# Performance work log

Hardware: AMD Instinct MI355X
Metric: run time of the kernel (lower is better)

Reference implementation:

```python
import jax, jax.numpy as jnp
import numpy as np

CP_SPACING = (4, 4, 4)
SIGMAS = tuple(0.44 * cp for cp in CP_SPACING)


def _gaussian_kernel_3d(sigmas):
    # Faithful to DeepReg layer_util.gaussian_filter_3d
    ks = [int(np.ceil(s * 3) + np.mod(np.ceil(s * 3) + 1, 2)) for s in sigmas]
    grid = np.stack(np.meshgrid(*[np.arange(k) for k in ks], indexing="ij"), axis=0)  # [3,k,k,k]
    mean = ((np.asarray(ks, np.float64) - 1.0) / 2.0).reshape(-1, 1, 1, 1)
    var = (np.asarray(sigmas, np.float64) ** 2.0).reshape(-1, 1, 1, 1)
    norm = 1.0 / (np.sqrt(2.0 * np.pi) ** 3 + np.prod(sigmas))  # as in DeepReg source
    kernel = norm * np.exp(-np.sum((grid - mean) ** 2.0 / (2.0 * var), axis=0))
    kernel = kernel / np.sum(kernel)  # sums to 1
    return kernel.astype(np.float32)  # [k,k,k]


def setup_inputs() -> dict:
    key = jax.random.key(0)
    image = jax.random.normal(key, (4, 160, 160, 160, 3), dtype=jnp.float32)  # DDF volume, 3 channels
    kernel = jnp.asarray(_gaussian_kernel_3d(SIGMAS))  # deterministic [7,7,7] Gaussian buffer
    return {"image": image, "kernel": kernel}


def reference(image, kernel):
    b, d1, d2, d3, c = image.shape
    # DeepReg's [k,k,k,3,3] diagonal kernel == depthwise blur per channel.
    kdw = jnp.tile(kernel[..., None, None], (1, 1, 1, 1, c))  # [k,k,k,1,C]
    blurred = jax.lax.conv_general_dilated(
        image, kdw,
        window_strides=(1, 1, 1),
        padding="SAME",
        dimension_numbers=("NDHWC", "DHWIO", "NDHWC"),
        feature_group_count=c,
    )
    # output control-point grid: ceil(dim / cp_spacing) + 3
    size = tuple(int(np.ceil(v / cp)) + 3 for v, cp in zip((d1, d2, d3), CP_SPACING))
    # tf.image.resize bilinear (TF2) uses half-pixel centers == jax.image.resize 'linear'
    out = jax.image.resize(blurred, (b,) + size + (c,), method="linear")
    return out
```

## Files before the change

### kernel.cpp

```cpp
#include <hip/hip_runtime.h>

#define NB 4
#define NI 160
#define NO 43
#define NC 3
#define KS 7
#define KPAD 3
#define MT 16
#define CH 8

#define ROWF (NI * NC)
#define PROW 132
#define PROW4 (PROW / 4)
#define LROW 484
#define SLICE (NO * NO * NC)

#define A1_BYTES ((size_t)NB * NI * NI * PROW * 4)
#define A2_BYTES ((size_t)NB * NI * NO * PROW * 4)
#define P2_THREADS ((size_t)NB * NI * NO * PROW4)
#define P3_THREADS ((size_t)NB * NO * NO * PROW4)

struct __align__(16) Tables {
    float wa3[NO][20];
    float w1[NO][MT];
    int   o1[NO][MT];
    int   o0[NO][MT];
    int   j3[NO];
    int   jlo[NO];
};

constexpr double ctaylor(double r) {
    double s = 1.0, term = 1.0;
    for (int n = 1; n <= 13; ++n) { term *= r / (double)n; s += term; }
    return s;
}
constexpr double cexp_neg(double x) {
    double y = -x;
    int k = (int)(y * 16.0);
    double r = y - (double)k / 16.0;
    double e16 = ctaylor(1.0 / 16.0);
    double p = 1.0;
    for (int i = 0; i < k; ++i) p *= e16;
    return 1.0 / (p * ctaylor(r));
}
constexpr int cceil(double x)  { int c = (int)x; return ((double)c < x) ? c + 1 : c; }
constexpr int cfloor(double x) { int f = (int)x; return ((double)f > x) ? f - 1 : f; }
constexpr double cabsd(double x) { return x < 0 ? -x : x; }

constexpr double comp_w(int j, double sf, int ilo, int ihi, const double* g) {
    if (j >= NI || j < 0) return 0.0;
    double cw = 0.0;
    for (int t = 0; t < KS; ++t) {
        int i = j + KPAD - t;
        if (i >= ilo && i <= ihi) {
            double w = 1.0 - cabsd(sf - (double)i) * (43.0 / 160.0);
            if (w > 0.0) cw += g[t] * w;
        }
    }
    return cw;
}

constexpr Tables make_tables() {
    Tables T{};
    double g[KS] = {};
    double gs = 0.0;
    const double sig = 0.44 * 4.0;
    for (int i = 0; i < KS; ++i) {
        double d = (double)i - 3.0;
        g[i] = cexp_neg(-(d * d) / (2.0 * sig * sig));
        gs += g[i];
    }
    for (int i = 0; i < KS; ++i) g[i] /= gs;

    const double inv_scale = 160.0 / 43.0;
    for (int o = 0; o < NO; ++o) {
        double sf = ((double)o + 0.5) * inv_scale - 0.5;
        int ilo = cceil(sf - inv_scale);  if (ilo < 0) ilo = 0;
        int ihi = cfloor(sf + inv_scale); if (ihi > NI - 1) ihi = NI - 1;
        double wsum = 0.0;
        for (int i = ilo; i <= ihi; ++i) {
            double w = 1.0 - cabsd(sf - (double)i) * (43.0 / 160.0);
            if (w > 0.0) wsum += w;
        }
        int jlo = ilo - KPAD; if (jlo < 0) jlo = 0;
        int j0 = jlo & ~3;
        T.j3[o] = j0;
        T.jlo[o] = jlo;
        for (int m = 0; m < 20; ++m)
            T.wa3[o][m] = (float)(comp_w(j0 + m, sf, ilo, ihi, g) / wsum);
        for (int k = 0; k < MT; ++k) {
            int j = jlo + k;
            T.w1[o][k] = (float)(comp_w(j, sf, ilo, ihi, g) / wsum);
            int jc = (j < NI) ? j : (NI - 1);
            T.o1[o][k] = jc * (PROW * 4);
            T.o0[o][k] = jc * (NO * PROW * 4);
        }
    }
    return T;
}

__constant__ Tables dT = make_tables();

__global__ __launch_bounds__(256, 4) void k_p1(
        const float* __restrict__ img, float* __restrict__ A1) {
    __shared__ __align__(16) float rows[8 * LROW + 64];
    __shared__ __align__(16) float swa[NO * 20];
    __shared__ int sj0[NO];
    int t = threadIdx.x;
    int blk = blockIdx.x;

    const float4* src = (const float4*)(img + (size_t)blk * (8 * ROWF));
    for (int gidx = t; gidx < 8 * ROWF / 4; gidx += 256) {
        int row = gidx / (ROWF / 4), m = gidx % (ROWF / 4);
        *(float4*)(rows + row * LROW + 4 * m) = src[gidx];
    }
    if (t < 32) rows[(t >> 2) * LROW + ROWF + (t & 3)] = 0.f;
    if (t < 64) rows[8 * LROW + t] = 0.f;
    for (int k = t; k < NO * 20; k += 256) swa[k] = ((const float*)dT.wa3)[k];
    if (t < NO) sj0[t] = dT.j3[t];
    __syncthreads();

    float* dst = A1 + (size_t)blk * (8 * PROW);
    for (int task = t; task < NO * 8; task += 256) {
        int o3 = task >> 3, row = task & 7;
        int j0 = sj0[o3];
        const float4* dp = (const float4*)(rows + row * LROW + 3 * j0);
        const float4* wp = (const float4*)(swa + o3 * 20);
        float d[60], wv[20];
        #pragma unroll
        for (int m = 0; m < 15; ++m) {
            float4 v = dp[m];
            d[4 * m + 0] = v.x; d[4 * m + 1] = v.y;
            d[4 * m + 2] = v.z; d[4 * m + 3] = v.w;
        }
        #pragma unroll
        for (int m = 0; m < 5; ++m) {
            float4 v = wp[m];
            wv[4 * m + 0] = v.x; wv[4 * m + 1] = v.y;
            wv[4 * m + 2] = v.z; wv[4 * m + 3] = v.w;
        }
        float a0 = 0.f, a1 = 0.f, a2 = 0.f;
        #pragma unroll
        for (int jj = 0; jj < 20; ++jj) {
            float w = wv[jj];
            a0 += w * d[3 * jj + 0];
            a1 += w * d[3 * jj + 1];
            a2 += w * d[3 * jj + 2];
        }
        float* op = dst + row * PROW + o3 * 3;
        op[0] = a0; op[1] = a1; op[2] = a2;
    }
    if (t < 8) {
        float* op = dst + t * PROW + NO * NC;
        op[0] = 0.f; op[1] = 0.f; op[2] = 0.f;
    }
}

__device__ __forceinline__ int xcd_swz(int wg, int nwg) {
    int q = nwg >> 3, r = nwg & 7;
    int x = wg & 7, i = wg >> 3;
    return (x < r ? x * (q + 1) : r * (q + 1) + (x - r) * q) + i;
}

__global__ __launch_bounds__(256) void k_p2(
        const float* __restrict__ A1, float* __restrict__ A2) {
    int blk = xcd_swz(blockIdx.x, gridDim.x);
    size_t idx = (size_t)blk * 256 + threadIdx.x;
    if (idx >= P2_THREADS) return;
    int ii = (int)idx;
    int col4 = ii % PROW4;
    int o2   = (ii / PROW4) % NO;
    int slab = ii / (PROW4 * NO);
    const char* base = (const char*)A1 + ((size_t)slab * NI * PROW + col4 * 4) * 4;
    const float4* wv = (const float4*)dT.w1[o2];
    const int4*   ov = (const int4*)dT.o1[o2];
    float4 w0 = wv[0], w1v = wv[1], w2 = wv[2], w3 = wv[3];
    int4   j0 = ov[0], j1 = ov[1], j2 = ov[2], j3 = ov[3];
    float4 a = {0.f, 0.f, 0.f, 0.f};
#define TAP4(J, W) { float4 v = *(const float4*)(base + (unsigned)(J)); \
                     a.x += (W) * v.x; a.y += (W) * v.y; a.z += (W) * v.z; a.w += (W) * v.w; }
    TAP4(j0.x, w0.x) TAP4(j0.y, w0.y) TAP4(j0.z, w0.z) TAP4(j0.w, w0.w)
    TAP4(j1.x, w1v.x) TAP4(j1.y, w1v.y) TAP4(j1.z, w1v.z) TAP4(j1.w, w1v.w)
    TAP4(j2.x, w2.x) TAP4(j2.y, w2.y) TAP4(j2.z, w2.z) TAP4(j2.w, w2.w)
    TAP4(j3.x, w3.x) TAP4(j3.y, w3.y) TAP4(j3.z, w3.z) TAP4(j3.w, w3.w)
#undef TAP4
    ((float4*)A2)[idx] = a;
}

__global__ __launch_bounds__(256) void k_p3(
        const float* __restrict__ A2, float* __restrict__ out) {
    int blk = xcd_swz(blockIdx.x, gridDim.x);
    size_t idx = (size_t)blk * 256 + threadIdx.x;
    if (idx >= P3_THREADS) return;
    int ii = (int)idx;
    int col4 = ii % PROW4;
    int o2   = (ii / PROW4) % NO;
    int o1   = (ii / (PROW4 * NO)) % NO;
    int b    = ii / (PROW4 * NO * NO);
    const char* base = (const char*)A2 +
        (((size_t)b * NI * NO + o2) * PROW + col4 * 4) * 4;
    const float4* wv = (const float4*)dT.w1[o1];
    const int4*   ov = (const int4*)dT.o0[o1];
    float4 w0 = wv[0], w1v = wv[1], w2 = wv[2], w3 = wv[3];
    int4   j0 = ov[0], j1 = ov[1], j2 = ov[2], j3 = ov[3];
    float4 a = {0.f, 0.f, 0.f, 0.f};
#define TAP4(J, W) { float4 v = *(const float4*)(base + (unsigned)(J)); \
                     a.x += (W) * v.x; a.y += (W) * v.y; a.z += (W) * v.z; a.w += (W) * v.w; }
    TAP4(j0.x, w0.x) TAP4(j0.y, w0.y) TAP4(j0.z, w0.z) TAP4(j0.w, w0.w)
    TAP4(j1.x, w1v.x) TAP4(j1.y, w1v.y) TAP4(j1.z, w1v.z) TAP4(j1.w, w1v.w)
    TAP4(j2.x, w2.x) TAP4(j2.y, w2.y) TAP4(j2.z, w2.z) TAP4(j2.w, w2.w)
    TAP4(j3.x, w3.x) TAP4(j3.y, w3.y) TAP4(j3.z, w3.z) TAP4(j3.w, w3.w)
#undef TAP4
    int tile = (b * NO + o1) * NO + o2;
    float* ob = out + (size_t)tile * (NO * NC) + col4 * 4;
    int col = col4 * 4;
    float av[4] = {a.x, a.y, a.z, a.w};
    #pragma unroll
    for (int e = 0; e < 4; ++e)
        if (col + e < NO * NC) ob[e] = av[e];
}

__global__ __launch_bounds__(256) void k_passA(
        const float* __restrict__ img, float* __restrict__ S) {
    __shared__ float rows[CH * NI * NC];
    __shared__ float T[CH * NO * NC];
    __shared__ float acc[NO * NO * NC];
    __shared__ float w2[NO * MT];
    __shared__ int   s2[NO];
    int t = threadIdx.x;
    int blk = blockIdx.x;
    const float* src = img + (size_t)blk * (NI * NI * NC);
    for (int k = t; k < NO * MT; k += 256) w2[k] = ((const float*)dT.w1)[k];
    for (int k = t; k < NO; k += 256) s2[k] = dT.jlo[k];
    for (int k = t; k < NO * NO * NC; k += 256) acc[k] = 0.f;
    __syncthreads();
    for (int chunk = 0; chunk < NI / CH; ++chunk) {
        const float4* csrc = (const float4*)(src + (size_t)chunk * CH * NI * NC);
        for (int k = t; k < CH * NI * NC / 4; k += 256)
            ((float4*)rows)[k] = csrc[k];
        __syncthreads();
        for (int task = t; task < CH * NO; task += 256) {
            int ch = task / NO, o3 = task % NO;
            int st = s2[o3];
            const float* rp = rows + ch * NI * NC;
            float a0 = 0.f, a1 = 0.f, a2 = 0.f;
            #pragma unroll
            for (int k = 0; k < MT; ++k) {
                int j = st + k; j = (j < NI) ? j : (NI - 1);
                float w = w2[o3 * MT + k];
                a0 += w * rp[j * 3 + 0];
                a1 += w * rp[j * 3 + 1];
                a2 += w * rp[j * 3 + 2];
            }
            T[task * NC + 0] = a0;
            T[task * NC + 1] = a1;
            T[task * NC + 2] = a2;
        }
        __syncthreads();
        int i2base = chunk * CH;
        for (int task = t; task < NO * NO; task += 256) {
            int o2 = task / NO, o3 = task % NO;
            int st = s2[o2];
            int k0 = i2base - st;        k0 = (k0 > 0) ? k0 : 0;
            int k1 = i2base + CH - st;   k1 = (k1 < MT) ? k1 : MT;
            if (k1 > k0) {
                float a0 = 0.f, a1 = 0.f, a2 = 0.f;
                for (int k = k0; k < k1; ++k) {
                    float w = w2[o2 * MT + k];
                    int ch = st + k - i2base;
                    a0 += w * T[(ch * NO + o3) * NC + 0];
                    a1 += w * T[(ch * NO + o3) * NC + 1];
                    a2 += w * T[(ch * NO + o3) * NC + 2];
                }
                acc[task * NC + 0] += a0;
                acc[task * NC + 1] += a1;
                acc[task * NC + 2] += a2;
            }
        }
        __syncthreads();
    }
    float* Sp = S + (size_t)blk * (NO * NO * NC);
    for (int k = t; k < NO * NO * NC; k += 256) Sp[k] = acc[k];
}

__global__ __launch_bounds__(256) void k_passB(
        const float* __restrict__ S, float* __restrict__ out) {
    int blk = blockIdx.x;
    int b = blk / NO, o1 = blk % NO;
    __shared__ float w1s[MT];
    __shared__ int s1v;
    if (threadIdx.x < MT) w1s[threadIdx.x] = dT.w1[o1][threadIdx.x];
    if (threadIdx.x == 0) s1v = dT.jlo[o1];
    __syncthreads();
    const float* Sb = S + (size_t)b * NI * (NO * NO * NC);
    float* ob = out + (size_t)blk * (NO * NO * NC);
    int st = s1v;
    for (int e = threadIdx.x; e < NO * NO * NC; e += 256) {
        float a = 0.f;
        #pragma unroll
        for (int k = 0; k < MT; ++k) {
            int i1 = st + k; i1 = (i1 < NI) ? i1 : (NI - 1);
            a += w1s[k] * Sb[(size_t)i1 * (NO * NO * NC) + e];
        }
        ob[e] = a;
    }
}

extern "C" void kernel_launch(void* const* d_in, const int* in_sizes, int n_in,
                              void* d_out, int out_size, void* d_ws, size_t ws_size,
                              hipStream_t stream) {
    (void)in_sizes; (void)n_in; (void)out_size;
    const float* img = (const float*)d_in[0];
    float* out = (float*)d_out;
    char* ws = (char*)d_ws;

    if (ws_size >= A1_BYTES + A2_BYTES) {
        float* A1 = (float*)ws;
        float* A2 = (float*)(ws + A1_BYTES);
        k_p1<<<NB * NI * (NI / 8), 256, 0, stream>>>(img, A1);
        int p2b = (int)((P2_THREADS + 255) / 256);
        k_p2<<<p2b, 256, 0, stream>>>(A1, A2);
        int p3b = (int)((P3_THREADS + 255) / 256);
        k_p3<<<p3b, 256, 0, stream>>>(A2, out);
    } else {
        float* S = (float*)ws;
        k_passA<<<NB * NI, 256, 0, stream>>>(img, S);
        k_passB<<<NB * NO, 256, 0, stream>>>(S, out);
    }
}
```

Baseline: 80.66 us.

## Fuse first two separable passes into one kernel using shared-memory row chunks

Merges the innermost-axis blur-resample pass and the middle-axis pass into one kernel. Each block handles one slab and half of the output rows, streaming 8-row chunks of input into shared memory, reducing along the innermost axis into a tile, then accumulating middle-axis taps in registers. This removes the large A1 intermediate buffer and its global write and read. In exchange, the grid has only 1280 blocks, each looping serially over chunks with two barriers per chunk, and the input rows covered by both halves are loaded and reduced twice.

```diff
diff --git a/kernel.cpp b/kernel.cpp
--- a/kernel.cpp
+++ b/kernel.cpp
@@ -15,15 +15,12 @@
 #define LROW 484
 #define SLICE (NO * NO * NC)
 
-#define A1_BYTES ((size_t)NB * NI * NI * PROW * 4)
 #define A2_BYTES ((size_t)NB * NI * NO * PROW * 4)
-#define P2_THREADS ((size_t)NB * NI * NO * PROW4)
 #define P3_THREADS ((size_t)NB * NO * NO * PROW4)
 
 struct __align__(16) Tables {
     float wa3[NO][20];
     float w1[NO][MT];
-    int   o1[NO][MT];
     int   o0[NO][MT];
     int   j3[NO];
     int   jlo[NO];
@@ -92,7 +89,6 @@
             int j = jlo + k;
             T.w1[o][k] = (float)(comp_w(j, sf, ilo, ihi, g) / wsum);
             int jc = (j < NI) ? j : (NI - 1);
-            T.o1[o][k] = jc * (PROW * 4);
             T.o0[o][k] = jc * (NO * PROW * 4);
         }
     }
@@ -101,90 +97,111 @@
 
 __constant__ Tables dT = make_tables();
 
-__global__ __launch_bounds__(256, 4) void k_p1(
-        const float* __restrict__ img, float* __restrict__ A1) {
-    __shared__ __align__(16) float rows[8 * LROW + 64];
+__global__ __launch_bounds__(256, 4) void k_f2(
+        const float* __restrict__ img, float* __restrict__ A2) {
+    __shared__ __align__(16) float raw[8 * LROW + 64];
+    __shared__ __align__(16) float tc[8 * PROW];
     __shared__ __align__(16) float swa[NO * 20];
-    __shared__ int sj0[NO];
-    int t = threadIdx.x;
-    int blk = blockIdx.x;
-
-    const float4* src = (const float4*)(img + (size_t)blk * (8 * ROWF));
-    for (int gidx = t; gidx < 8 * ROWF / 4; gidx += 256) {
-        int row = gidx / (ROWF / 4), m = gidx % (ROWF / 4);
-        *(float4*)(rows + row * LROW + 4 * m) = src[gidx];
-    }
-    if (t < 32) rows[(t >> 2) * LROW + ROWF + (t & 3)] = 0.f;
-    if (t < 64) rows[8 * LROW + t] = 0.f;
+    __shared__ __align__(16) float sw1[NO * MT];
+    __shared__ int sj0[NO], sjlo[NO];
+    const int t = threadIdx.x;
+    const int blk = blockIdx.x;
+    const int slab = blk >> 1;
+    const int half = blk & 1;
+    const int o2a = half ? 22 : 0;
+    const int o2n = half ? 21 : 22;
+
+    const float4* src4 = (const float4*)(img + (size_t)slab * (NI * ROWF));
+
     for (int k = t; k < NO * 20; k += 256) swa[k] = ((const float*)dT.wa3)[k];
-    if (t < NO) sj0[t] = dT.j3[t];
+    for (int k = t; k < NO * MT; k += 256) sw1[k] = ((const float*)dT.w1)[k];
+    if (t < NO) { sj0[t] = dT.j3[t]; sjlo[t] = dT.jlo[t]; }
+    if (t < 32) raw[(t >> 2) * LROW + ROWF + (t & 3)] = 0.f;
+    if (t >= 32 && t < 96) raw[8 * LROW + (t - 32)] = 0.f;
+    if (t >= 96 && t < 120) {
+        int q = t - 96;
+        tc[(q / 3) * PROW + NO * NC + (q % 3)] = 0.f;
+    }
+
+    const int r0 = dT.jlo[o2a];
+    int r1 = dT.jlo[o2a + o2n - 1] + MT; if (r1 > NI) r1 = NI;
+    const int nc = (r1 - r0 + 7) >> 3;
+
+    float4 acc0 = {0.f,0.f,0.f,0.f}, acc1 = acc0, acc2 = acc0;
+    const int lim = o2n * PROW4;
+    const int idx0 = t, idx1 = t + 256, idx2 = t + 512;
+    const int o2_0 = o2a + idx0 / PROW4, c4_0 = idx0 % PROW4;
+    const int o2_1 = o2a + idx1 / PROW4, c4_1 = idx1 % PROW4;
+    const int o2_2 = (idx2 < lim) ? (o2a + idx2 / PROW4) : o2a;
+    const int c4_2 = idx2 % PROW4;
+
+    for (int g = t; g < 960; g += 256) {
+        int row = g / 120, m = g % 120;
+        int grow = r0 + row; grow = (grow < NI) ? grow : (NI - 1);
+        *(float4*)(raw + row * LROW + 4 * m) = src4[(size_t)grow * 120 + m];
+    }
     __syncthreads();
 
-    float* dst = A1 + (size_t)blk * (8 * PROW);
-    for (int task = t; task < NO * 8; task += 256) {
-        int o3 = task >> 3, row = task & 7;
-        int j0 = sj0[o3];
-        const float4* dp = (const float4*)(rows + row * LROW + 3 * j0);
-        const float4* wp = (const float4*)(swa + o3 * 20);
-        float d[60], wv[20];
-        #pragma unroll
-        for (int m = 0; m < 15; ++m) {
-            float4 v = dp[m];
-            d[4 * m + 0] = v.x; d[4 * m + 1] = v.y;
-            d[4 * m + 2] = v.z; d[4 * m + 3] = v.w;
-        }
-        #pragma unroll
-        for (int m = 0; m < 5; ++m) {
-            float4 v = wp[m];
-            wv[4 * m + 0] = v.x; wv[4 * m + 1] = v.y;
-            wv[4 * m + 2] = v.z; wv[4 * m + 3] = v.w;
-        }
-        float a0 = 0.f, a1 = 0.f, a2 = 0.f;
-        #pragma unroll
-        for (int jj = 0; jj < 20; ++jj) {
-            float w = wv[jj];
-            a0 += w * d[3 * jj + 0];
-            a1 += w * d[3 * jj + 1];
-            a2 += w * d[3 * jj + 2];
-        }
-        float* op = dst + row * PROW + o3 * 3;
-        op[0] = a0; op[1] = a1; op[2] = a2;
-    }
-    if (t < 8) {
-        float* op = dst + t * PROW + NO * NC;
-        op[0] = 0.f; op[1] = 0.f; op[2] = 0.f;
-    }
+    for (int c = 0; c < nc; ++c) {
+        const int cs = r0 + 8 * c;
+        for (int task = t; task < 8 * NO; task += 256) {
+            int row = task & 7, o3 = task >> 3;
+            int j0 = sj0[o3];
+            const float4* dp = (const float4*)(raw + row * LROW + 3 * j0);
+            const float4* wp = (const float4*)(swa + o3 * 20);
+            float a0 = 0.f, a1 = 0.f, a2 = 0.f;
+            #pragma unroll
+            for (int m = 0; m < 5; ++m) {
+                float4 w4 = wp[m];
+                float4 v0 = dp[3 * m], v1 = dp[3 * m + 1], v2 = dp[3 * m + 2];
+                a0 += w4.x * v0.x; a1 += w4.x * v0.y; a2 += w4.x * v0.z;
+                a0 += w4.y * v0.w; a1 += w4.y * v1.x; a2 += w4.y * v1.y;
+                a0 += w4.z * v1.z; a1 += w4.z * v1.w; a2 += w4.z * v2.x;
+                a0 += w4.w * v2.y; a1 += w4.w * v2.z; a2 += w4.w * v2.w;
+            }
+            float* op = tc + row * PROW + o3 * 3;
+            op[0] = a0; op[1] = a1; op[2] = a2;
+        }
+        __syncthreads();
+
+        if (c + 1 < nc) {
+            const int ns = cs + 8;
+            for (int g = t; g < 960; g += 256) {
+                int row = g / 120, m = g % 120;
+                int grow = ns + row; grow = (grow < NI) ? grow : (NI - 1);
+                *(float4*)(raw + row * LROW + 4 * m) = src4[(size_t)grow * 120 + m];
+            }
+        }
+
+#define ACC(ACCV, O2, C4) {                                                    \
+            int jl = sjlo[O2];                                                 \
+            int k0 = cs - jl;        if (k0 < 0) k0 = 0;                       \
+            int k1 = cs + 8 - jl;    if (k1 > MT) k1 = MT;                     \
+            int km = NI - jl;        if (k1 > km) k1 = km;                     \
+            for (int k = k0; k < k1; ++k) {                                    \
+                float w = sw1[(O2) * MT + k];                                  \
+                const float4 v = *(const float4*)(&tc[(jl + k - cs) * PROW + (C4) * 4]); \
+                ACCV.x += w * v.x; ACCV.y += w * v.y;                          \
+                ACCV.z += w * v.z; ACCV.w += w * v.w;                          \
+            }                                                                  \
+        }
+        ACC(acc0, o2_0, c4_0)
+        ACC(acc1, o2_1, c4_1)
+        if (idx2 < lim) ACC(acc2, o2_2, c4_2)
+#undef ACC
+        __syncthreads();
+    }
+
+    float4* dst = (float4*)A2 + (size_t)slab * (NO * PROW4) + o2a * PROW4;
+    dst[idx0] = acc0;
+    dst[idx1] = acc1;
+    if (idx2 < lim) dst[idx2] = acc2;
 }
 
 __device__ __forceinline__ int xcd_swz(int wg, int nwg) {
     int q = nwg >> 3, r = nwg & 7;
     int x = wg & 7, i = wg >> 3;
     return (x < r ? x * (q + 1) : r * (q + 1) + (x - r) * q) + i;
-}
-
-__global__ __launch_bounds__(256) void k_p2(
-        const float* __restrict__ A1, float* __restrict__ A2) {
-    int blk = xcd_swz(blockIdx.x, gridDim.x);
-    size_t idx = (size_t)blk * 256 + threadIdx.x;
-    if (idx >= P2_THREADS) return;
-    int ii = (int)idx;
-    int col4 = ii % PROW4;
-    int o2   = (ii / PROW4) % NO;
-    int slab = ii / (PROW4 * NO);
-    const char* base = (const char*)A1 + ((size_t)slab * NI * PROW + col4 * 4) * 4;
-    const float4* wv = (const float4*)dT.w1[o2];
-    const int4*   ov = (const int4*)dT.o1[o2];
-    float4 w0 = wv[0], w1v = wv[1], w2 = wv[2], w3 = wv[3];
-    int4   j0 = ov[0], j1 = ov[1], j2 = ov[2], j3 = ov[3];
-    float4 a = {0.f, 0.f, 0.f, 0.f};
-#define TAP4(J, W) { float4 v = *(const float4*)(base + (unsigned)(J)); \
-                     a.x += (W) * v.x; a.y += (W) * v.y; a.z += (W) * v.z; a.w += (W) * v.w; }
-    TAP4(j0.x, w0.x) TAP4(j0.y, w0.y) TAP4(j0.z, w0.z) TAP4(j0.w, w0.w)
-    TAP4(j1.x, w1v.x) TAP4(j1.y, w1v.y) TAP4(j1.z, w1v.z) TAP4(j1.w, w1v.w)
-    TAP4(j2.x, w2.x) TAP4(j2.y, w2.y) TAP4(j2.z, w2.z) TAP4(j2.w, w2.w)
-    TAP4(j3.x, w3.x) TAP4(j3.y, w3.y) TAP4(j3.z, w3.z) TAP4(j3.w, w3.w)
-#undef TAP4
-    ((float4*)A2)[idx] = a;
 }
 
 __global__ __launch_bounds__(256) void k_p3(
@@ -314,12 +331,9 @@
     float* out = (float*)d_out;
     char* ws = (char*)d_ws;
 
-    if (ws_size >= A1_BYTES + A2_BYTES) {
-        float* A1 = (float*)ws;
-        float* A2 = (float*)(ws + A1_BYTES);
-        k_p1<<<NB * NI * (NI / 8), 256, 0, stream>>>(img, A1);
-        int p2b = (int)((P2_THREADS + 255) / 256);
-        k_p2<<<p2b, 256, 0, stream>>>(A1, A2);
+    if (ws_size >= A2_BYTES) {
+        float* A2 = (float*)ws;
+        k_f2<<<NB * NI * 2, 256, 0, stream>>>(img, A2);
         int p3b = (int)((P3_THREADS + 255) / 256);
         k_p3<<<p3b, 256, 0, stream>>>(A2, out);
     } else {
```

After: 97.46 us. 1.21x slower.
